# Kernel tuning notes

Measured on AMD Instinct MI355X. Metric: run time of the kernel, lower is better.

The kernel has to match this reference:

```python
import jax, jax.numpy as jnp
import numpy as np

N = 20000        # atoms
NEIGH = 12       # neighbors per atom
BSTEPS = 40      # bond GBF steps, range [0, 8]
ASTEPS = 20      # angle GBF steps, range [-1, 1]
H = 64           # hidden size
NCLS = 2         # n_classification
NCRYS = 20       # crystals (contiguous blocks of 1000 atoms)
NREL = 3         # edge relation types


def gbf(data, dmin, dmax, steps):
    # Gaussian basis expansion: exp(-(d - mu)^2 / gamma^2), gamma = (max-min)/steps
    filters = jnp.linspace(dmin, dmax, steps)
    gamma = (dmax - dmin) / steps
    return jnp.exp(-((data[..., None] - filters) ** 2) / gamma ** 2)


def rgcn(x, src, dst, etype, W_rel, W_root, b):
    # RGCNConv (PyG default): out = x @ W_root + b + sum_r mean_{j in N_r(i)} x_j @ W_r
    out = x @ W_root + b
    for r in range(NREL):
        w = (etype == r).astype(x.dtype)                     # [E]
        msg = (x @ W_rel[r])[src] * w[:, None]               # transform-then-gather: [E, H]
        s = jax.ops.segment_sum(msg, dst, num_segments=x.shape[0])
        c = jax.ops.segment_sum(w, dst, num_segments=x.shape[0])
        out = out + s / jnp.maximum(c, 1.0)[:, None]
    return out


def _forward(bond_fea, angle_fea, species, nbr_idx, crys_idx,
             W1b_rel, W1b_root, b1b, W1a_rel, W1a_root, b1a,
             W2b_rel, W2b_root, b2b, W2a_rel, W2a_root, b2a,
             fc_W, fc_b):
    n = bond_fea.shape[0]
    src = jnp.repeat(jnp.arange(n, dtype=jnp.int32), NEIGH)  # edge sources
    dst = nbr_idx.reshape(-1)                                # edge targets
    etype = species[src] + species[dst]                      # 0/1/2 per species pair

    edge_fea = gbf(bond_fea, 0.0, 8.0, BSTEPS).reshape(n, -1)      # [N, 480]
    ang_fea = gbf(angle_fea, -1.0, 1.0, ASTEPS).reshape(n, -1)     # [N, 2880]

    bf = jax.nn.relu(rgcn(edge_fea, src, dst, etype, W1b_rel, W1b_root, b1b))
    af = jax.nn.relu(rgcn(ang_fea, src, dst, etype, W1a_rel, W1a_root, b1a))
    # dropout treated as identity (eval/deterministic reference)
    bf = jax.nn.relu(rgcn(bf, src, dst, etype, W2b_rel, W2b_root, b2b))
    af = jax.nn.relu(rgcn(af, src, dst, etype, W2a_rel, W2a_root, b2a))

    feat = jnp.concatenate([bf, af], axis=1)                 # [N, 128]

    # pool: mean over contiguous [start, end) ranges per crystal
    starts = crys_idx[:, 0]
    crys_id = jnp.searchsorted(starts, jnp.arange(n), side='right') - 1
    sums = jax.ops.segment_sum(feat, crys_id, num_segments=NCRYS)
    counts = (crys_idx[:, 1] - crys_idx[:, 0]).astype(feat.dtype)[:, None]
    pooled = sums / counts                                   # [NCRYS, 128]

    return pooled @ fc_W + fc_b                              # [NCRYS, NCLS]


def setup_inputs() -> dict:
    key = jax.random.key(0)
    ks = jax.random.split(key, 20)
    bond_fea = jax.random.uniform(ks[0], (N, NEIGH), dtype=jnp.float32) * 8.0
    angle_fea = jax.random.uniform(ks[1], (N, NEIGH, NEIGH), dtype=jnp.float32) * 2.0 - 1.0
    species = jax.random.randint(ks[2], (N,), 0, 2, dtype=jnp.int32)
    nbr_idx = jax.random.randint(ks[3], (N, NEIGH), 0, N, dtype=jnp.int32)
    starts = jnp.arange(NCRYS, dtype=jnp.int32) * (N // NCRYS)
    crys_idx = jnp.stack([starts, starts + (N // NCRYS)], axis=1)

    def w(k, shape, fan_in):
        return jax.random.normal(k, shape, dtype=jnp.float32) / np.sqrt(fan_in)

    in_b = BSTEPS * NEIGH            # 480
    in_a = ASTEPS * NEIGH * NEIGH    # 2880
    return {
        'bond_fea': bond_fea, 'angle_fea': angle_fea, 'species': species,
        'nbr_idx': nbr_idx, 'crys_idx': crys_idx,
        'W1b_rel': w(ks[4], (NREL, in_b, H), in_b), 'W1b_root': w(ks[5], (in_b, H), in_b),
        'b1b': jnp.zeros((H,), jnp.float32),
        'W1a_rel': w(ks[6], (NREL, in_a, H), in_a), 'W1a_root': w(ks[7], (in_a, H), in_a),
        'b1a': jnp.zeros((H,), jnp.float32),
        'W2b_rel': w(ks[8], (NREL, H, H), H), 'W2b_root': w(ks[9], (H, H), H),
        'b2b': jnp.zeros((H,), jnp.float32),
        'W2a_rel': w(ks[10], (NREL, H, H), H), 'W2a_root': w(ks[11], (H, H), H),
        'b2a': jnp.zeros((H,), jnp.float32),
        'fc_W': w(ks[12], (2 * H, NCLS), 2 * H), 'fc_b': jnp.zeros((NCLS,), jnp.float32),
    }


def reference(bond_fea, angle_fea, species, nbr_idx, crys_idx,
              W1b_rel, W1b_root, b1b, W1a_rel, W1a_root, b1a,
              W2b_rel, W2b_root, b2b, W2a_rel, W2a_root, b2a,
              fc_W, fc_b):
    return _forward(bond_fea, angle_fea, species, nbr_idx, crys_idx,
                    W1b_rel, W1b_root, b1b, W1a_rel, W1a_root, b1a,
                    W2b_rel, W2b_root, b2b, W2a_rel, W2a_root, b2a,
                    fc_W, fc_b)
```

## Files before the change

kernel.cpp:

```cpp
#include <hip/hip_runtime.h>

#define NN 20000
#define NNP 20096
#define NEIGH 12
#define NCRYS 20
#define MT2 1256
#define NSUB 16

typedef __bf16 bf16x8 __attribute__((ext_vector_type(8)));
typedef __bf16 bf16x4 __attribute__((ext_vector_type(4)));
typedef __bf16 bf16x2 __attribute__((ext_vector_type(2)));
typedef float f32x4 __attribute__((ext_vector_type(4)));

__device__ __forceinline__ float readlane_f(float v, int l) {
    return __int_as_float(__builtin_amdgcn_readlane(__float_as_int(v), l));
}

__device__ __forceinline__ void pack8(const float* Wrel, const float* Wroot,
                                      __bf16* Wp, int K, int t) {
    int n = t & 255, kq = t >> 8;
    int kt = kq >> 2, k8 = kq & 3;
    int r = n >> 6, h = n & 63;
    int k0 = kt * 32 + k8 * 8;
    const float* src = (r < 3) ? (Wrel + ((size_t)r * K + k0) * 64 + h)
                               : (Wroot + (size_t)k0 * 64 + h);
    bf16x8 v;
#pragma unroll
    for (int j = 0; j < 8; ++j) v[j] = (__bf16)src[(size_t)j * 64];
    size_t off = (((((size_t)kt * 16 + (n >> 4)) * 4 + k8) * 16) + (n & 15)) * 8;
    *(bf16x8*)&Wp[off] = v;
}

__device__ __forceinline__ void pack_cat8(const float* Wrel, const float* Wroot,
                                          __bf16* Wp, int t) {
    int n = t & 63, kq = t >> 6;
    int kt = kq >> 2, k8 = kq & 3;
    int k0 = kt * 32 + k8 * 8;
    int q = k0 >> 6, kk = k0 & 63;
    const float* src = q ? (Wrel + (((size_t)(q - 1) * 64 + kk) * 64) + n)
                         : (Wroot + (size_t)kk * 64 + n);
    bf16x8 v;
#pragma unroll
    for (int j = 0; j < 8; ++j) v[j] = (__bf16)src[(size_t)j * 64];
    size_t off = (((((size_t)kt * 4 + (n >> 4)) * 4 + k8) * 16) + (n & 15)) * 8;
    *(bf16x8*)&Wp[off] = v;
}

__global__ __launch_bounds__(256) void setup_kernel(
    const int* __restrict__ species, const int* __restrict__ nbr,
    int* __restrict__ adj, int* __restrict__ deg,
    const float* __restrict__ W1b_rel, const float* __restrict__ W1b_root,
    const float* __restrict__ W1a_rel, const float* __restrict__ W1a_root,
    const float* __restrict__ W2b_rel, const float* __restrict__ W2b_root,
    const float* __restrict__ W2a_rel, const float* __restrict__ W2a_root,
    __bf16* __restrict__ Wp1b, __bf16* __restrict__ Wp1a,
    __bf16* __restrict__ Wp2b, __bf16* __restrict__ Wp2a,
    const float* __restrict__ bond, const float* __restrict__ angle,
    float* __restrict__ bondT, float* __restrict__ angleT) {
    __shared__ float ls[64 * 145];
    const int bx = blockIdx.x, tid = threadIdx.x;
    if (bx < 938) {
        int e = bx * 256 + tid;
        if (e < NN * NEIGH) {
            int i = e / NEIGH;
            int d = nbr[e];
            int r = species[i] + species[d];
            int slot = atomicAdd(&deg[d], 1);
            if (slot < 64) adj[(size_t)d * 64 + slot] = i | (r << 28);
        }
    } else if (bx < 938 + 256) {
        const int S0 = 15360;
        const int S1 = S0 + 92160;
        const int S2 = S1 + 2048;
        const int S3 = S2 + 2048;
        const int S4 = S3 + 8192;
        const int S5 = S4 + 49152;
        for (int idx = (bx - 938) * 256 + tid; idx < S5; idx += 256 * 256) {
            if (idx < S0)       pack8(W1b_rel, W1b_root, Wp1b, 480, idx);
            else if (idx < S1)  pack8(W1a_rel, W1a_root, Wp1a, 2880, idx - S0);
            else if (idx < S2)  pack_cat8(W2b_rel, W2b_root, Wp2b, idx - S1);
            else if (idx < S3)  pack_cat8(W2a_rel, W2a_root, Wp2a, idx - S2);
            else if (idx < S4)  Wp1b[480 * 256 + (idx - S3)] = (__bf16)0.f;
            else                Wp1a[2880 * 256 + (idx - S4)] = (__bf16)0.f;
        }
    } else {
        int tb = bx - 1194;
        if (tb < 314) {
            int m0 = tb * 64;
            for (int idx = tid; idx < 64 * 144; idx += 256) {
                int mm = idx / 144, j = idx - mm * 144;
                int m = m0 + mm;
                ls[mm * 145 + j] = (m < NN) ? angle[(size_t)m * 144 + j] : 0.f;
            }
            __syncthreads();
            for (int idx = tid; idx < 156 * 64; idx += 256) {
                int j = idx >> 6, mm = idx & 63;
                angleT[(size_t)j * NNP + m0 + mm] = (j < 144) ? ls[mm * 145 + j] : 0.f;
            }
        } else {
            int m0 = (tb - 314) * 64;
            for (int idx = tid; idx < 64 * 12; idx += 256) {
                int mm = idx / 12, j = idx - mm * 12;
                int m = m0 + mm;
                ls[mm * 13 + j] = (m < NN) ? bond[(size_t)m * 12 + j] : 0.f;
            }
            __syncthreads();
            for (int idx = tid; idx < 16 * 64; idx += 256) {
                int j = idx >> 6, mm = idx & 63;
                bondT[(size_t)j * NNP + m0 + mm] = (j < 12) ? ls[mm * 13 + j] : 0.f;
            }
        }
    }
}

template <int MODE>
__device__ __forceinline__ void gemm1_body(const float* __restrict__ xT,
                                           const __bf16* __restrict__ Wp,
                                           __bf16* __restrict__ Y, int mb,
                                           __bf16* __restrict__ Al,
                                           int ph0, int nph) {
    constexpr int DIVN = (MODE == 0) ? 40 : 20;
    constexpr int ADDJ = 64 / DIVN;
    constexpr int ADDS = 64 % DIVN;
    constexpr float F0 = (MODE == 0) ? 0.f : -1.f;
    constexpr float FS = (MODE == 0) ? (8.f / 39.f) : (2.f / 19.f);
    constexpr float NG2 = ((MODE == 0) ? -25.f : -100.f) * 1.44269504f;
    const float C  = __builtin_amdgcn_exp2f(2.f * NG2 * FS * FS);
    const float P1 = NG2 * FS * FS;
    const float P2 = -2.f * NG2 * FS;

    const int tid = threadIdx.x;
    const int lane = tid & 63, wv = tid >> 6;
    const int m0 = mb * 64;
    const int smt = tid >> 7;
    const int sk8 = (tid >> 5) & 3;
    const int smi = (tid >> 1) & 15;
    const int sjh = (tid & 1) * 4;
    const int sgm = m0 + smt * 16 + smi;
    const int kk0 = sk8 * 8 + sjh;
    const int swoff = (((smt * 4 + sk8) * 16 + smi) * 8 + sjh);
    const int k8b = lane >> 4, nib = lane & 15;

    f32x4 acc[4][2] = {};

    const int k00 = ph0 * 64 + kk0;
    const int k01 = ph0 * 64 + 32 + kk0;
    const float* pA0 = xT + (size_t)(k00 / DIVN) * NNP + sgm;
    const float* pA1 = xT + (size_t)(k01 / DIVN) * NNP + sgm;
    int sL0 = k00 % DIVN, sL1 = k01 % DIVN;
    int sS0 = sL0, sS1 = sL1;

    const bf16x8* pB0 = (const bf16x8*)Wp + (size_t)ph0 * 2048 +
                        ((size_t)(2 * wv) * 4 + k8b) * 16 + nib;
    const bf16x8* pB1 = pB0 + 1024;

    bf16x8 bEv[4], bOd[4];

    auto advL = [&]() {
        sL0 += ADDS;
        if (sL0 >= DIVN) { sL0 -= DIVN; pA0 += (size_t)(ADDJ + 1) * NNP; } else pA0 += (size_t)ADDJ * NNP;
        sL1 += ADDS;
        if (sL1 >= DIVN) { sL1 -= DIVN; pA1 += (size_t)(ADDJ + 1) * NNP; } else pA1 += (size_t)ADDJ * NNP;
    };
    auto advS = [&]() {
        sS0 += ADDS; if (sS0 >= DIVN) sS0 -= DIVN;
        sS1 += ADDS; if (sS1 >= DIVN) sS1 -= DIVN;
    };
    auto loadB = [&](bf16x8* d) {
        d[0] = pB0[0]; d[1] = pB0[64]; d[2] = pB1[0]; d[3] = pB1[64];
        pB0 += 2048; pB1 += 2048;
    };
    auto stage = [&](float a0, float a1, __bf16* dst) {
        float d0 = a0 - (F0 + (float)sS0 * FS);
        float d1 = a1 - (F0 + (float)sS1 * FS);
        float e0a = __builtin_amdgcn_exp2f(NG2 * d0 * d0);
        float q0a = __builtin_amdgcn_exp2f(fmaf(P2, d0, P1));
        float e0b = __builtin_amdgcn_exp2f(NG2 * d1 * d1);
        float q0b = __builtin_amdgcn_exp2f(fmaf(P2, d1, P1));
        float e1a = e0a * q0a, q1a = q0a * C;
        float e2a = e1a * q1a, e3a = e2a * q1a * C;
        float e1b = e0b * q0b, q1b = q0b * C;
        float e2b = e1b * q1b, e3b = e2b * q1b * C;
        bf16x4 v0, v1;
        v0[0] = (__bf16)e0a; v0[1] = (__bf16)e1a; v0[2] = (__bf16)e2a; v0[3] = (__bf16)e3a;
        v1[0] = (__bf16)e0b; v1[1] = (__bf16)e1b; v1[2] = (__bf16)e2b; v1[3] = (__bf16)e3b;
        *(bf16x4*)&dst[swoff] = v0;
        *(bf16x4*)&dst[2048 + swoff] = v1;
    };
    auto mma = [&](const __bf16* Ab, const bf16x8* bc) {
        bf16x8 af[4], ag[4];
#pragma unroll
        for (int t4 = 0; t4 < 4; ++t4) {
            af[t4] = *(const bf16x8*)&Ab[(((((t4 << 2) + k8b) << 4) + nib) << 3)];
            ag[t4] = *(const bf16x8*)&Ab[2048 + (((((t4 << 2) + k8b) << 4) + nib) << 3)];
        }
#pragma unroll
        for (int i = 0; i < 4; ++i) {
            acc[i][0] = __builtin_amdgcn_mfma_f32_16x16x32_bf16(af[i], bc[0], acc[i][0], 0, 0, 0);
            acc[i][1] = __builtin_amdgcn_mfma_f32_16x16x32_bf16(af[i], bc[1], acc[i][1], 0, 0, 0);
        }
#pragma unroll
        for (int i = 0; i < 4; ++i) {
            acc[i][0] = __builtin_amdgcn_mfma_f32_16x16x32_bf16(ag[i], bc[2], acc[i][0], 0, 0, 0);
            acc[i][1] = __builtin_amdgcn_mfma_f32_16x16x32_bf16(ag[i], bc[3], acc[i][1], 0, 0, 0);
        }
    };

    float a00 = pA0[0], a01 = pA1[0]; advL();
    float aN0 = pA0[0], aN1 = pA1[0]; advL();
    stage(a00, a01, Al); advS();
    loadB(bEv);
    loadB(bOd);
    __syncthreads();

    const int np2 = nph >> 1;
    for (int p2 = 0; p2 < np2; ++p2) {
        const bool last = (p2 == np2 - 1);
        mma(Al, bEv);
        if (!last) loadB(bEv);
        stage(aN0, aN1, Al + 4096); advS();
        if (!last) { aN0 = pA0[0]; aN1 = pA1[0]; advL(); }
        __syncthreads();
        mma(Al + 4096, bOd);
        if (!last) {
            loadB(bOd);
            stage(aN0, aN1, Al); advS();
            aN0 = pA0[0]; aN1 = pA1[0]; advL();
        }
        __syncthreads();
    }

    const int mrow0 = m0 + ((lane >> 4) << 2);
    const int ncol = (wv << 5) + nib;
#pragma unroll
    for (int i = 0; i < 4; ++i)
#pragma unroll
        for (int j = 0; j < 2; ++j)
#pragma unroll
            for (int v = 0; v < 4; ++v) {
                int m = mrow0 + i * 16 + v;
                if (m < NN) Y[(size_t)m * 256 + ncol + j * 16] = (__bf16)acc[i][j][v];
            }
}

__global__ __launch_bounds__(512, 4) void mega_gemm1(const float* __restrict__ bondT,
                                                     const float* __restrict__ angleT,
                                                     const __bf16* __restrict__ Wp1b,
                                                     const __bf16* __restrict__ Wp1a,
                                                     __bf16* __restrict__ Yb,
                                                     __bf16* __restrict__ Ya1,
                                                     __bf16* __restrict__ Ya2) {
    __shared__ __align__(16) __bf16 Al[2 * 4096];
    int bx = blockIdx.x;
    if (bx < 628) {
        int half = bx & 1, mb = bx >> 1;
        gemm1_body<1>(angleT, Wp1a, half ? Ya2 : Ya1, mb, Al, half ? 24 : 0, 24);
    } else {
        gemm1_body<0>(bondT, Wp1b, Yb, bx - 628, Al, 0, 8);
    }
}

__global__ __launch_bounds__(256) void agg1(const __bf16* __restrict__ Yb,
                                            const __bf16* __restrict__ Ya1,
                                            const __bf16* __restrict__ Ya2,
                                            const int* __restrict__ adj,
                                            const int* __restrict__ deg,
                                            const float* __restrict__ biasb,
                                            const float* __restrict__ biasa,
                                            __bf16* __restrict__ Hba) {
    int node = blockIdx.x * 4 + (threadIdx.x >> 6);
    int h = threadIdx.x & 63;
    if (node >= NN) return;
    int dg = min(deg[node], 64);
    int e = adj[(size_t)node * 64 + h];
    bool val = h < dg;
    int r = e >> 28;
    unsigned long long bl0 = __ballot(val && r == 0);
    unsigned long long bl1 = __ballot(val && r == 1);
    unsigned long long bl2 = __ballot(val && r == 2);
    int c0 = __popcll(bl0), c1 = __popcll(bl1), c2 = __popcll(bl2);
    float w = val ? 1.f / (float)((r == 0) ? c0 : (r == 1) ? c1 : c2) : 0.f;
    float sb = 0.f, sa = 0.f;
    if (dg > 0) {
        int e0 = __builtin_amdgcn_readfirstlane(e);
        int ec = val ? e : e0;
        for (int k0 = 0; k0 < dg; k0 += 16) {
            float vb[16], va[16];
#pragma unroll
            for (int i = 0; i < 16; ++i) {
                int ek = __builtin_amdgcn_readlane(ec, k0 + i);
                size_t base = (size_t)(ek & 0x0FFFFFFF) * 256 + (ek >> 28) * 64 + h;
                vb[i] = (float)Yb[base];
                va[i] = (float)Ya1[base] + (float)Ya2[base];
            }
#pragma unroll
            for (int i = 0; i < 16; ++i) {
                float wk = readlane_f(w, k0 + i);
                sb = fmaf(vb[i], wk, sb);
                sa = fmaf(va[i], wk, sa);
            }
        }
    }
    size_t ro = (size_t)node * 256 + 192 + h;
    float ob = (float)Yb[ro] + biasb[h] + sb;
    float oa = (float)Ya1[ro] + (float)Ya2[ro] + biasa[h] + sa;
    bf16x2 o;
    o[0] = (__bf16)fmaxf(ob, 0.f);
    o[1] = (__bf16)fmaxf(oa, 0.f);
    *(bf16x2*)(Hba + ((size_t)node * 64 + h) * 2) = o;
}

__global__ __launch_bounds__(256) void agg2(const __bf16* __restrict__ Hba,
                                            const int* __restrict__ adj,
                                            const int* __restrict__ deg,
                                            __bf16* __restrict__ Xb,
                                            __bf16* __restrict__ Xa) {
    int node = blockIdx.x * 4 + (threadIdx.x >> 6);
    int h = threadIdx.x & 63;
    float hb = 0.f, rb0 = 0.f, rb1 = 0.f, rb2 = 0.f;
    float ha = 0.f, ra0 = 0.f, ra1 = 0.f, ra2 = 0.f;
    if (node < NN) {
        int dg = min(deg[node], 64);
        int e = adj[(size_t)node * 64 + h];
        bool val = h < dg;
        int r = e >> 28;
        unsigned long long bl0 = __ballot(val && r == 0);
        unsigned long long bl1 = __ballot(val && r == 1);
        unsigned long long bl2 = __ballot(val && r == 2);
        int c0 = __popcll(bl0), c1 = __popcll(bl1), c2 = __popcll(bl2);
        float sb0 = 0.f, sb1 = 0.f, sb2 = 0.f;
        float sa0 = 0.f, sa1 = 0.f, sa2 = 0.f;
        bf16x2 hr = *(const bf16x2*)(Hba + ((size_t)node * 64 + h) * 2);
        hb = (float)hr[0];
        ha = (float)hr[1];
        if (dg > 0) {
            int e0 = __builtin_amdgcn_readfirstlane(e);
            int ec = val ? e : e0;
            for (int k0 = 0; k0 < dg; k0 += 16) {
                float vb[16], va[16];
#pragma unroll
                for (int i = 0; i < 16; ++i) {
                    int ek = __builtin_amdgcn_readlane(ec, k0 + i);
                    bf16x2 v2 = *(const bf16x2*)(Hba + (((size_t)(ek & 0x0FFFFFFF)) * 64 + h) * 2);
                    vb[i] = (float)v2[0];
                    va[i] = (float)v2[1];
                }
#pragma unroll
                for (int i = 0; i < 16; ++i) {
                    int kk = k0 + i;
                    if (kk < dg) {
                        int rr = __builtin_amdgcn_readlane(ec, kk) >> 28;
                        if (rr == 0)      { sb0 += vb[i]; sa0 += va[i]; }
                        else if (rr == 1) { sb1 += vb[i]; sa1 += va[i]; }
                        else              { sb2 += vb[i]; sa2 += va[i]; }
                    }
                }
            }
        }
        float i0 = 1.f / fmaxf((float)c0, 1.f);
        float i1 = 1.f / fmaxf((float)c1, 1.f);
        float i2 = 1.f / fmaxf((float)c2, 1.f);
        rb0 = sb0 * i0; rb1 = sb1 * i1; rb2 = sb2 * i2;
        ra0 = sa0 * i0; ra1 = sa1 * i1; ra2 = sa2 * i2;
    }
    float vb4[4] = {hb, rb0, rb1, rb2};
    float va4[4] = {ha, ra0, ra1, ra2};
    size_t rowb = (size_t)node * 256 + h;
#pragma unroll
    for (int q = 0; q < 4; ++q) {
        Xb[rowb + q * 64] = (__bf16)vb4[q];
        Xa[rowb + q * 64] = (__bf16)va4[q];
    }
}

__global__ __launch_bounds__(256) void gemm3(const __bf16* __restrict__ Xb,
                                             const __bf16* __restrict__ Xa,
                                             const __bf16* __restrict__ Wpb,
                                             const __bf16* __restrict__ Wpa,
                                             const float* __restrict__ bb,
                                             const float* __restrict__ ba,
                                             const int* __restrict__ crys,
                                             float* __restrict__ pooled) {
    const int ch = blockIdx.y;
    const __bf16* X = ch ? Xa : Xb;
    const bf16x8* Bg = (const bf16x8*)(ch ? Wpa : Wpb);
    const float* bias = ch ? ba : bb;
    const int base = ch ? 64 : 0;
    const int tid = threadIdx.x, lane = tid & 63, wv = tid >> 6;
    const int mt0 = blockIdx.x * 8 + wv * 2;
    const int k8b = lane >> 4, nib = lane & 15;
    const __bf16* pA0 = X + ((size_t)(mt0 * 16 + nib)) * 256 + k8b * 8;
    const __bf16* pA1 = pA0 + 16 * 256;
    f32x4 acc[2][4] = {};
#pragma unroll
    for (int kt = 0; kt < 8; ++kt) {
        bf16x8 a0 = *(const bf16x8*)(pA0 + kt * 32);
        bf16x8 a1 = *(const bf16x8*)(pA1 + kt * 32);
        bf16x8 b0 = Bg[(((size_t)kt * 4 + 0) * 4 + k8b) * 16 + nib];
        bf16x8 b1 = Bg[(((size_t)kt * 4 + 1) * 4 + k8b) * 16 + nib];
        bf16x8 b2 = Bg[(((size_t)kt * 4 + 2) * 4 + k8b) * 16 + nib];
        bf16x8 b3 = Bg[(((size_t)kt * 4 + 3) * 4 + k8b) * 16 + nib];
        acc[0][0] = __builtin_amdgcn_mfma_f32_16x16x32_bf16(a0, b0, acc[0][0], 0, 0, 0);
        acc[0][1] = __builtin_amdgcn_mfma_f32_16x16x32_bf16(a0, b1, acc[0][1], 0, 0, 0);
        acc[0][2] = __builtin_amdgcn_mfma_f32_16x16x32_bf16(a0, b2, acc[0][2], 0, 0, 0);
        acc[0][3] = __builtin_amdgcn_mfma_f32_16x16x32_bf16(a0, b3, acc[0][3], 0, 0, 0);
        acc[1][0] = __builtin_amdgcn_mfma_f32_16x16x32_bf16(a1, b0, acc[1][0], 0, 0, 0);
        acc[1][1] = __builtin_amdgcn_mfma_f32_16x16x32_bf16(a1, b1, acc[1][1], 0, 0, 0);
        acc[1][2] = __builtin_amdgcn_mfma_f32_16x16x32_bf16(a1, b2, acc[1][2], 0, 0, 0);
        acc[1][3] = __builtin_amdgcn_mfma_f32_16x16x32_bf16(a1, b3, acc[1][3], 0, 0, 0);
    }
    const int rowoff = ((lane >> 4) << 2);
#pragma unroll
    for (int i = 0; i < 2; ++i)
#pragma unroll
        for (int v = 0; v < 4; ++v) {
            int m = (mt0 + i) * 16 + rowoff + v;
            if (m < NN) {
                int cc = 0;
#pragma unroll
                for (int t = 1; t < NCRYS; ++t) cc += (m >= crys[t * 2]) ? 1 : 0;
                int sub = ((m >> 4) + ((m >> 2) & 3)) & (NSUB - 1);
                float* pb = &pooled[((size_t)cc * NSUB + sub) * 128 + base];
#pragma unroll
                for (int j = 0; j < 4; ++j) {
                    int n = j * 16 + nib;
                    float o = fmaxf(acc[i][j][v] + bias[n], 0.f);
                    atomicAdd(&pb[n], o);
                }
            }
        }
}

__global__ void final2(const float* __restrict__ pooled, const int* __restrict__ crys,
                       const float* __restrict__ fcW, const float* __restrict__ fcb,
                       float* __restrict__ out) {
    int c = blockIdx.x >> 1, o = blockIdx.x & 1;
    int l = threadIdx.x;
    float cnt = (float)(crys[c * 2 + 1] - crys[c * 2]);
    float sb = 0.f, sa = 0.f;
    for (int s = 0; s < NSUB; ++s) {
        sb += pooled[((size_t)c * NSUB + s) * 128 + l];
        sa += pooled[((size_t)c * NSUB + s) * 128 + 64 + l];
    }
    float a = sb * fcW[l * 2 + o] + sa * fcW[(64 + l) * 2 + o];
    for (int s = 32; s > 0; s >>= 1) a += __shfl_down(a, s);
    if (l == 0) out[c * 2 + o] = a / cnt + fcb[o];
}

extern "C" void kernel_launch(void* const* d_in, const int* in_sizes, int n_in,
                              void* d_out, int out_size, void* d_ws, size_t ws_size,
                              hipStream_t stream) {
    const float* bond    = (const float*)d_in[0];
    const float* angle   = (const float*)d_in[1];
    const int*   species = (const int*)d_in[2];
    const int*   nbr     = (const int*)d_in[3];
    const int*   crys    = (const int*)d_in[4];
    const float* W1b_rel = (const float*)d_in[5];
    const float* W1b_root= (const float*)d_in[6];
    const float* b1b     = (const float*)d_in[7];
    const float* W1a_rel = (const float*)d_in[8];
    const float* W1a_root= (const float*)d_in[9];
    const float* b1a     = (const float*)d_in[10];
    const float* W2b_rel = (const float*)d_in[11];
    const float* W2b_root= (const float*)d_in[12];
    const float* b2b     = (const float*)d_in[13];
    const float* W2a_rel = (const float*)d_in[14];
    const float* W2a_root= (const float*)d_in[15];
    const float* b2a     = (const float*)d_in[16];
    const float* fcW     = (const float*)d_in[17];
    const float* fcb     = (const float*)d_in[18];
    float* out = (float*)d_out;

    char* ws = (char*)d_ws;
    size_t off = 0;
    auto alloc = [&](size_t bytes) {
        char* p = ws + off;
        off = (off + bytes + 255) & ~(size_t)255;
        return p;
    };
    __bf16* Wp1b = (__bf16*)alloc((size_t)512 * 256 * 2);
    __bf16* Wp1a = (__bf16*)alloc((size_t)3072 * 256 * 2);
    __bf16* Wp2b = (__bf16*)alloc((size_t)256 * 64 * 2);
    __bf16* Wp2a = (__bf16*)alloc((size_t)256 * 64 * 2);
    float*  bondT = (float*)alloc((size_t)16 * NNP * 4);
    float*  angleT= (float*)alloc((size_t)156 * NNP * 4);
    __bf16* Yb   = (__bf16*)alloc((size_t)NN * 256 * 2);
    __bf16* Ya1  = (__bf16*)alloc((size_t)NN * 256 * 2);
    __bf16* Ya2  = (__bf16*)alloc((size_t)NN * 256 * 2);
    __bf16* Hba  = (__bf16*)alloc((size_t)NNP * 64 * 2 * 2);
    __bf16* Xb   = (__bf16*)alloc((size_t)NNP * 256 * 2);
    __bf16* Xa   = (__bf16*)alloc((size_t)NNP * 256 * 2);
    int*    adj  = (int*)alloc((size_t)NN * 64 * 4);
    int*    deg  = (int*)alloc((size_t)NN * 4);
    float*  pooled = (float*)alloc((size_t)NCRYS * NSUB * 128 * 4);

    hipMemsetAsync(deg, 0, (size_t)NN * 4, stream);
    hipMemsetAsync(pooled, 0, (size_t)NCRYS * NSUB * 128 * 4, stream);

    setup_kernel<<<1822, 256, 0, stream>>>(species, nbr, adj, deg,
                                           W1b_rel, W1b_root, W1a_rel, W1a_root,
                                           W2b_rel, W2b_root, W2a_rel, W2a_root,
                                           Wp1b, Wp1a, Wp2b, Wp2a,
                                           bond, angle, bondT, angleT);

    mega_gemm1<<<942, 512, 0, stream>>>(bondT, angleT, Wp1b, Wp1a, Yb, Ya1, Ya2);
    agg1<<<5000, 256, 0, stream>>>(Yb, Ya1, Ya2, adj, deg, b1b, b1a, Hba);
    agg2<<<5024, 256, 0, stream>>>(Hba, adj, deg, Xb, Xa);
    gemm3<<<dim3(157, 2), 256, 0, stream>>>(Xb, Xa, Wp2b, Wp2a, b2b, b2a, crys, pooled);
    final2<<<NCRYS * 2, 64, 0, stream>>>(pooled, crys, fcW, fcb, out);
}
```

Baseline: 223.9 us.

## Fuse second-layer aggregation with the pooling GEMM through shared memory

Merges agg2 and gemm3 into a single kernel. Each block aggregates 16 nodes into an LDS tile and then runs MFMA on that tile, with pooling done by atomics. This removes the global write and re-read of the Xb/Xa intermediates (about 20 MB) and one kernel launch. In exchange the GEMM phase is narrower, with 16 rows per block, and each wave serializes aggregation over 4 nodes.

```diff
diff --git a/kernel.cpp b/kernel.cpp
--- a/kernel.cpp
+++ b/kernel.cpp
@@ -4,7 +4,6 @@
 #define NNP 20096
 #define NEIGH 12
 #define NCRYS 20
-#define MT2 1256
 #define NSUB 16
 
 typedef __bf16 bf16x8 __attribute__((ext_vector_type(8)));
@@ -310,125 +309,112 @@
     *(bf16x2*)(Hba + ((size_t)node * 64 + h) * 2) = o;
 }
 
-__global__ __launch_bounds__(256) void agg2(const __bf16* __restrict__ Hba,
-                                            const int* __restrict__ adj,
-                                            const int* __restrict__ deg,
-                                            __bf16* __restrict__ Xb,
-                                            __bf16* __restrict__ Xa) {
-    int node = blockIdx.x * 4 + (threadIdx.x >> 6);
-    int h = threadIdx.x & 63;
-    float hb = 0.f, rb0 = 0.f, rb1 = 0.f, rb2 = 0.f;
-    float ha = 0.f, ra0 = 0.f, ra1 = 0.f, ra2 = 0.f;
-    if (node < NN) {
-        int dg = min(deg[node], 64);
-        int e = adj[(size_t)node * 64 + h];
-        bool val = h < dg;
-        int r = e >> 28;
-        unsigned long long bl0 = __ballot(val && r == 0);
-        unsigned long long bl1 = __ballot(val && r == 1);
-        unsigned long long bl2 = __ballot(val && r == 2);
-        int c0 = __popcll(bl0), c1 = __popcll(bl1), c2 = __popcll(bl2);
-        float sb0 = 0.f, sb1 = 0.f, sb2 = 0.f;
-        float sa0 = 0.f, sa1 = 0.f, sa2 = 0.f;
-        bf16x2 hr = *(const bf16x2*)(Hba + ((size_t)node * 64 + h) * 2);
-        hb = (float)hr[0];
-        ha = (float)hr[1];
-        if (dg > 0) {
-            int e0 = __builtin_amdgcn_readfirstlane(e);
-            int ec = val ? e : e0;
-            for (int k0 = 0; k0 < dg; k0 += 16) {
-                float vb[16], va[16];
-#pragma unroll
-                for (int i = 0; i < 16; ++i) {
-                    int ek = __builtin_amdgcn_readlane(ec, k0 + i);
-                    bf16x2 v2 = *(const bf16x2*)(Hba + (((size_t)(ek & 0x0FFFFFFF)) * 64 + h) * 2);
-                    vb[i] = (float)v2[0];
-                    va[i] = (float)v2[1];
-                }
-#pragma unroll
-                for (int i = 0; i < 16; ++i) {
-                    int kk = k0 + i;
-                    if (kk < dg) {
-                        int rr = __builtin_amdgcn_readlane(ec, kk) >> 28;
-                        if (rr == 0)      { sb0 += vb[i]; sa0 += va[i]; }
-                        else if (rr == 1) { sb1 += vb[i]; sa1 += va[i]; }
-                        else              { sb2 += vb[i]; sa2 += va[i]; }
+__global__ __launch_bounds__(256) void agg2mm(const __bf16* __restrict__ Hba,
+                                              const int* __restrict__ adj,
+                                              const int* __restrict__ deg,
+                                              const __bf16* __restrict__ Wpb,
+                                              const __bf16* __restrict__ Wpa,
+                                              const float* __restrict__ bb,
+                                              const float* __restrict__ ba,
+                                              const int* __restrict__ crys,
+                                              float* __restrict__ pooled) {
+    __shared__ __align__(16) __bf16 Xl[2][16][264];
+    const int tid = threadIdx.x, lane = tid & 63, wv = tid >> 6;
+    const int node0 = blockIdx.x * 16;
+    const int h = lane;
+
+    for (int s = 0; s < 4; ++s) {
+        const int nl = wv * 4 + s;
+        const int node = node0 + nl;
+        float hb = 0.f, rb0 = 0.f, rb1 = 0.f, rb2 = 0.f;
+        float ha = 0.f, ra0 = 0.f, ra1 = 0.f, ra2 = 0.f;
+        if (node < NN) {
+            int dg = min(deg[node], 64);
+            int e = adj[(size_t)node * 64 + h];
+            bool val = h < dg;
+            int r = e >> 28;
+            unsigned long long bl0 = __ballot(val && r == 0);
+            unsigned long long bl1 = __ballot(val && r == 1);
+            unsigned long long bl2 = __ballot(val && r == 2);
+            int c0 = __popcll(bl0), c1 = __popcll(bl1), c2 = __popcll(bl2);
+            float sb0 = 0.f, sb1 = 0.f, sb2 = 0.f;
+            float sa0 = 0.f, sa1 = 0.f, sa2 = 0.f;
+            bf16x2 hr = *(const bf16x2*)(Hba + ((size_t)node * 64 + h) * 2);
+            hb = (float)hr[0];
+            ha = (float)hr[1];
+            if (dg > 0) {
+                int e0 = __builtin_amdgcn_readfirstlane(e);
+                int ec = val ? e : e0;
+                for (int k0 = 0; k0 < dg; k0 += 16) {
+                    float vb[16], va[16];
+#pragma unroll
+                    for (int i = 0; i < 16; ++i) {
+                        int ek = __builtin_amdgcn_readlane(ec, k0 + i);
+                        bf16x2 v2 = *(const bf16x2*)(Hba + (((size_t)(ek & 0x0FFFFFFF)) * 64 + h) * 2);
+                        vb[i] = (float)v2[0];
+                        va[i] = (float)v2[1];
+                    }
+#pragma unroll
+                    for (int i = 0; i < 16; ++i) {
+                        int kk = k0 + i;
+                        if (kk < dg) {
+                            int rr = __builtin_amdgcn_readlane(ec, kk) >> 28;
+                            if (rr == 0)      { sb0 += vb[i]; sa0 += va[i]; }
+                            else if (rr == 1) { sb1 += vb[i]; sa1 += va[i]; }
+                            else              { sb2 += vb[i]; sa2 += va[i]; }
+                        }
                     }
                 }
             }
-        }
-        float i0 = 1.f / fmaxf((float)c0, 1.f);
-        float i1 = 1.f / fmaxf((float)c1, 1.f);
-        float i2 = 1.f / fmaxf((float)c2, 1.f);
-        rb0 = sb0 * i0; rb1 = sb1 * i1; rb2 = sb2 * i2;
-        ra0 = sa0 * i0; ra1 = sa1 * i1; ra2 = sa2 * i2;
-    }
-    float vb4[4] = {hb, rb0, rb1, rb2};
-    float va4[4] = {ha, ra0, ra1, ra2};
-    size_t rowb = (size_t)node * 256 + h;
-#pragma unroll
-    for (int q = 0; q < 4; ++q) {
-        Xb[rowb + q * 64] = (__bf16)vb4[q];
-        Xa[rowb + q * 64] = (__bf16)va4[q];
-    }
-}
-
-__global__ __launch_bounds__(256) void gemm3(const __bf16* __restrict__ Xb,
-                                             const __bf16* __restrict__ Xa,
-                                             const __bf16* __restrict__ Wpb,
-                                             const __bf16* __restrict__ Wpa,
-                                             const float* __restrict__ bb,
-                                             const float* __restrict__ ba,
-                                             const int* __restrict__ crys,
-                                             float* __restrict__ pooled) {
-    const int ch = blockIdx.y;
-    const __bf16* X = ch ? Xa : Xb;
+            float i0 = 1.f / fmaxf((float)c0, 1.f);
+            float i1 = 1.f / fmaxf((float)c1, 1.f);
+            float i2 = 1.f / fmaxf((float)c2, 1.f);
+            rb0 = sb0 * i0; rb1 = sb1 * i1; rb2 = sb2 * i2;
+            ra0 = sa0 * i0; ra1 = sa1 * i1; ra2 = sa2 * i2;
+        }
+        float vb4[4] = {hb, rb0, rb1, rb2};
+        float va4[4] = {ha, ra0, ra1, ra2};
+#pragma unroll
+        for (int q = 0; q < 4; ++q) {
+            Xl[0][nl][q * 64 + h] = (__bf16)vb4[q];
+            Xl[1][nl][q * 64 + h] = (__bf16)va4[q];
+        }
+    }
+    __syncthreads();
+
+    const int ch = wv >> 1, colh = wv & 1;
+    const __bf16* Xc = &Xl[ch][0][0];
     const bf16x8* Bg = (const bf16x8*)(ch ? Wpa : Wpb);
     const float* bias = ch ? ba : bb;
     const int base = ch ? 64 : 0;
-    const int tid = threadIdx.x, lane = tid & 63, wv = tid >> 6;
-    const int mt0 = blockIdx.x * 8 + wv * 2;
     const int k8b = lane >> 4, nib = lane & 15;
-    const __bf16* pA0 = X + ((size_t)(mt0 * 16 + nib)) * 256 + k8b * 8;
-    const __bf16* pA1 = pA0 + 16 * 256;
-    f32x4 acc[2][4] = {};
+    f32x4 acc[2] = {};
 #pragma unroll
     for (int kt = 0; kt < 8; ++kt) {
-        bf16x8 a0 = *(const bf16x8*)(pA0 + kt * 32);
-        bf16x8 a1 = *(const bf16x8*)(pA1 + kt * 32);
-        bf16x8 b0 = Bg[(((size_t)kt * 4 + 0) * 4 + k8b) * 16 + nib];
-        bf16x8 b1 = Bg[(((size_t)kt * 4 + 1) * 4 + k8b) * 16 + nib];
-        bf16x8 b2 = Bg[(((size_t)kt * 4 + 2) * 4 + k8b) * 16 + nib];
-        bf16x8 b3 = Bg[(((size_t)kt * 4 + 3) * 4 + k8b) * 16 + nib];
-        acc[0][0] = __builtin_amdgcn_mfma_f32_16x16x32_bf16(a0, b0, acc[0][0], 0, 0, 0);
-        acc[0][1] = __builtin_amdgcn_mfma_f32_16x16x32_bf16(a0, b1, acc[0][1], 0, 0, 0);
-        acc[0][2] = __builtin_amdgcn_mfma_f32_16x16x32_bf16(a0, b2, acc[0][2], 0, 0, 0);
-        acc[0][3] = __builtin_amdgcn_mfma_f32_16x16x32_bf16(a0, b3, acc[0][3], 0, 0, 0);
-        acc[1][0] = __builtin_amdgcn_mfma_f32_16x16x32_bf16(a1, b0, acc[1][0], 0, 0, 0);
-        acc[1][1] = __builtin_amdgcn_mfma_f32_16x16x32_bf16(a1, b1, acc[1][1], 0, 0, 0);
-        acc[1][2] = __builtin_amdgcn_mfma_f32_16x16x32_bf16(a1, b2, acc[1][2], 0, 0, 0);
-        acc[1][3] = __builtin_amdgcn_mfma_f32_16x16x32_bf16(a1, b3, acc[1][3], 0, 0, 0);
+        bf16x8 a0 = *(const bf16x8*)&Xc[nib * 264 + kt * 32 + k8b * 8];
+        bf16x8 b0 = Bg[(((size_t)kt * 4 + colh * 2 + 0) * 4 + k8b) * 16 + nib];
+        bf16x8 b1 = Bg[(((size_t)kt * 4 + colh * 2 + 1) * 4 + k8b) * 16 + nib];
+        acc[0] = __builtin_amdgcn_mfma_f32_16x16x32_bf16(a0, b0, acc[0], 0, 0, 0);
+        acc[1] = __builtin_amdgcn_mfma_f32_16x16x32_bf16(a0, b1, acc[1], 0, 0, 0);
     }
     const int rowoff = ((lane >> 4) << 2);
 #pragma unroll
-    for (int i = 0; i < 2; ++i)
-#pragma unroll
-        for (int v = 0; v < 4; ++v) {
-            int m = (mt0 + i) * 16 + rowoff + v;
-            if (m < NN) {
-                int cc = 0;
-#pragma unroll
-                for (int t = 1; t < NCRYS; ++t) cc += (m >= crys[t * 2]) ? 1 : 0;
-                int sub = ((m >> 4) + ((m >> 2) & 3)) & (NSUB - 1);
-                float* pb = &pooled[((size_t)cc * NSUB + sub) * 128 + base];
-#pragma unroll
-                for (int j = 0; j < 4; ++j) {
-                    int n = j * 16 + nib;
-                    float o = fmaxf(acc[i][j][v] + bias[n], 0.f);
-                    atomicAdd(&pb[n], o);
-                }
-            }
-        }
+    for (int v = 0; v < 4; ++v) {
+        int m = node0 + rowoff + v;
+        if (m < NN) {
+            int cc = 0;
+#pragma unroll
+            for (int t = 1; t < NCRYS; ++t) cc += (m >= crys[t * 2]) ? 1 : 0;
+            int sub = ((m >> 4) + ((m >> 2) & 3)) & (NSUB - 1);
+            float* pb = &pooled[((size_t)cc * NSUB + sub) * 128 + base];
+#pragma unroll
+            for (int j = 0; j < 2; ++j) {
+                int n = colh * 32 + j * 16 + nib;
+                float o = fmaxf(acc[j][v] + bias[n], 0.f);
+                atomicAdd(&pb[n], o);
+            }
+        }
+    }
 }
 
 __global__ void final2(const float* __restrict__ pooled, const int* __restrict__ crys,
@@ -488,8 +474,6 @@
     __bf16* Ya1  = (__bf16*)alloc((size_t)NN * 256 * 2);
     __bf16* Ya2  = (__bf16*)alloc((size_t)NN * 256 * 2);
     __bf16* Hba  = (__bf16*)alloc((size_t)NNP * 64 * 2 * 2);
-    __bf16* Xb   = (__bf16*)alloc((size_t)NNP * 256 * 2);
-    __bf16* Xa   = (__bf16*)alloc((size_t)NNP * 256 * 2);
     int*    adj  = (int*)alloc((size_t)NN * 64 * 4);
     int*    deg  = (int*)alloc((size_t)NN * 4);
     float*  pooled = (float*)alloc((size_t)NCRYS * NSUB * 128 * 4);
@@ -505,7 +489,6 @@
 
     mega_gemm1<<<942, 512, 0, stream>>>(bondT, angleT, Wp1b, Wp1a, Yb, Ya1, Ya2);
     agg1<<<5000, 256, 0, stream>>>(Yb, Ya1, Ya2, adj, deg, b1b, b1a, Hba);
-    agg2<<<5024, 256, 0, stream>>>(Hba, adj, deg, Xb, Xa);
-    gemm3<<<dim3(157, 2), 256, 0, stream>>>(Xb, Xa, Wp2b, Wp2a, b2b, b2a, crys, pooled);
+    agg2mm<<<1256, 256, 0, stream>>>(Hba, adj, deg, Wp2b, Wp2a, b2b, b2a, crys, pooled);
     final2<<<NCRYS * 2, 64, 0, stream>>>(pooled, crys, fcW, fcb, out);
 }
```

Result: faster. 214.1 us (-4.4%).
